# Kernel optimization log

Hardware: AMD Instinct MI355X
Metric: run time of the kernel (lower is better)

## Reference

```python
import jax, jax.numpy as jnp
import numpy as np

N = 100000
E = 3200000
D_IN = 83
D_HID = 1024
N_CLASSES = 25


def setup_inputs() -> dict:
    key = jax.random.key(0)
    ks = jax.random.split(key, 10)
    feature = jax.random.normal(ks[0], (N, D_IN), dtype=jnp.float32)
    edge_row = jax.random.randint(ks[1], (E,), 0, N, dtype=jnp.int32)
    edge_col = jax.random.randint(ks[2], (E,), 0, N, dtype=jnp.int32)
    adj_val = jax.random.uniform(ks[3], (E,), dtype=jnp.float32)
    # Conv1d(1 -> 4, kernel 5, pad 2): weight [out=4, in=1, k=5]
    conv_w = jax.random.normal(ks[4], (4, 1, 5), dtype=jnp.float32) * 0.2
    conv_b = jnp.zeros((4,), dtype=jnp.float32)
    # GCN weights (kaiming-uniform-like scale), zero biases
    W1 = jax.random.uniform(ks[5], (D_IN, D_HID), dtype=jnp.float32,
                            minval=-1.0, maxval=1.0) * np.sqrt(6.0 / D_IN)
    b1 = jnp.zeros((D_HID,), dtype=jnp.float32)
    W2 = jax.random.uniform(ks[6], (D_HID, N_CLASSES), dtype=jnp.float32,
                            minval=-1.0, maxval=1.0) * np.sqrt(6.0 / D_HID)
    b2 = jnp.zeros((N_CLASSES,), dtype=jnp.float32)
    return {"feature": feature, "conv_w": conv_w, "conv_b": conv_b,
            "W1": W1, "b1": b1, "W2": W2, "b2": b2,
            "adj_val": adj_val, "edge_row": edge_row, "edge_col": edge_col}


def _spmm(vals, row, col, X):
    # sparse(adj) @ X : gather source rows, scale by edge value, scatter-add to dest
    return jax.ops.segment_sum(vals[:, None] * X[col], row, num_segments=N)


def reference(feature, conv_w, conv_b, W1, b1, W2, b2, adj_val, edge_row, edge_col):
    # Conv1d prelude: [N,1,83] -> [N,4,83], sum over channels, relu -> [N,83]
    x = jax.lax.conv_general_dilated(
        feature[:, None, :], conv_w, window_strides=(1,), padding=[(2, 2)],
        dimension_numbers=("NCH", "OIH", "NCH"))
    x = x + conv_b[None, :, None]
    x = jax.nn.relu(jnp.sum(x, axis=1))
    # GCN layer 1: relu(A @ (x W1) + b1)
    h = jax.nn.relu(_spmm(adj_val, edge_row, edge_col, x @ W1) + b1)
    # GCN layer 2: A @ (h W2) + b2
    logits = _spmm(adj_val, edge_row, edge_col, h @ W2) + b2
    return logits
```

## Files before the change

kernel.cpp:

```cpp
#include <hip/hip_runtime.h>

#define NN   100000
#define EE   3200000
#define DIN  83
#define DHID 1024
#define NCLS 25
#define XPAD 96
#define ZPAD 32

#define NBK     391
#define CHUNK   8192

typedef __attribute__((__ext_vector_type__(8))) short sh8;
typedef __attribute__((__ext_vector_type__(4))) float f4_t;

static __device__ __forceinline__ float relu_(float v) { return v > 0.f ? v : 0.f; }

static __device__ __forceinline__ unsigned short f2bf(float f) {
  unsigned int u = __float_as_uint(f);
  unsigned int r = u + 0x7FFFu + ((u >> 16) & 1u);
  return (unsigned short)(r >> 16);
}
static __device__ __forceinline__ float bflo(unsigned int q) {
  return __uint_as_float(q << 16);
}
static __device__ __forceinline__ float bfhi(unsigned int q) {
  return __uint_as_float(q & 0xFFFF0000u);
}

__global__ __launch_bounds__(256) void conv_relu_k(
    const float* __restrict__ feature, const float* __restrict__ conv_w,
    const float* __restrict__ conv_b, unsigned short* __restrict__ x) {
  float ws0 = conv_w[0] + conv_w[5] + conv_w[10] + conv_w[15];
  float ws1 = conv_w[1] + conv_w[6] + conv_w[11] + conv_w[16];
  float ws2 = conv_w[2] + conv_w[7] + conv_w[12] + conv_w[17];
  float ws3 = conv_w[3] + conv_w[8] + conv_w[13] + conv_w[18];
  float ws4 = conv_w[4] + conv_w[9] + conv_w[14] + conv_w[19];
  float bs  = conv_b[0] + conv_b[1] + conv_b[2] + conv_b[3];
  int t = blockIdx.x * 256 + threadIdx.x;
  if (t >= NN * 12) return;
  int n = t / 12;
  int g = t - n * 12;
  int i0 = g * 8;
  const float* f = feature + (size_t)n * DIN;
  float fv[12];
#pragma unroll
  for (int k = 0; k < 12; ++k) {
    int idx = i0 - 2 + k;
    fv[k] = (idx >= 0 && idx < DIN) ? f[idx] : 0.f;
  }
  sh8 vout;
#pragma unroll
  for (int j = 0; j < 8; ++j) {
    int i = i0 + j;
    unsigned short o = 0;
    if (i < DIN) {
      float acc = bs + ws0 * fv[j] + ws1 * fv[j + 1] + ws2 * fv[j + 2] +
                  ws3 * fv[j + 3] + ws4 * fv[j + 4];
      o = f2bf(relu_(acc));
    }
    vout[j] = (short)o;
  }
  *(sh8*)&x[(size_t)n * XPAD + i0] = vout;
}

__global__ void prep_k(const float* __restrict__ W1, unsigned short* __restrict__ w1t,
                       const float* __restrict__ W2, unsigned short* __restrict__ w2t,
                       int* __restrict__ gbk) {
  int idx = blockIdx.x * blockDim.x + threadIdx.x;
  if (idx < DHID * XPAD) {
    int k = idx / DHID;
    int n = idx - k * DHID;
    float v = (k < DIN) ? W1[k * DHID + n] : 0.f;
    w1t[n * XPAD + k] = f2bf(v);
  }
  if (idx < 32 * DHID) {
    int k = idx / 32;
    int n = idx - k * 32;
    float v = (n < NCLS) ? W2[k * NCLS + n] : 0.f;
    w2t[n * DHID + k] = f2bf(v);
  }
  if (idx < NBK * 16) gbk[idx] = 0;
}


__global__ __launch_bounds__(512) void bucket_hist_k(
    const int* __restrict__ row, int* __restrict__ gbk) {
  __shared__ int cnt[NBK];
  const int tid = threadIdx.x;
  for (int b = tid; b < NBK; b += 512) cnt[b] = 0;
  __syncthreads();
  const int cb = blockIdx.x * CHUNK;
  const int csize = (cb + CHUNK <= EE) ? CHUNK : (EE - cb);
  for (int i = tid; i < csize; i += 512)
    atomicAdd(&cnt[row[cb + i] >> 8], 1);
  __syncthreads();
  for (int b = tid; b < NBK; b += 512)
    if (cnt[b]) atomicAdd(&gbk[b * 16], cnt[b]);
}

__global__ void scan_buckets_k(const int* __restrict__ gbk,
                               int* __restrict__ bbase, int* __restrict__ gcur) {
  __shared__ int sd[512];
  int t = threadIdx.x;
  int v = (t < NBK) ? gbk[t * 16] : 0;
  sd[t] = v;
  __syncthreads();
  for (int off = 1; off < 512; off <<= 1) {
    int add = (t >= off) ? sd[t - off] : 0;
    __syncthreads();
    sd[t] += add;
    __syncthreads();
  }
  if (t < NBK) {
    int excl = sd[t] - v;
    bbase[t] = excl;
    gcur[t * 16] = excl;
  }
  if (t == 0) bbase[NBK] = EE;
}

__global__ __launch_bounds__(256) void partition_k(
    const float* __restrict__ vals, const int* __restrict__ row,
    const int* __restrict__ col, int* __restrict__ gcur,
    int2* __restrict__ tmp) {
  __shared__ int cnt[NBK];
  __shared__ int lcur[NBK];
  const int tid = threadIdx.x;
  const int cb = blockIdx.x * CHUNK;
  const int csize = (cb + CHUNK <= EE) ? CHUNK : (EE - cb);

  for (int b = tid; b < NBK; b += 256) cnt[b] = 0;
  __syncthreads();
  for (int i = tid; i < csize; i += 256)
    atomicAdd(&cnt[row[cb + i] >> 8], 1);
  __syncthreads();
  for (int b = tid; b < NBK; b += 256)
    lcur[b] = cnt[b] ? atomicAdd(&gcur[b * 16], cnt[b]) : 0;
  __syncthreads();
  for (int i = tid; i < csize; i += 256) {
    int r = row[cb + i];
    int pos = atomicAdd(&lcur[r >> 8], 1);
    tmp[pos] = make_int2(col[cb + i] | ((r & 255) << 17),
                         __float_as_int(vals[cb + i]));
  }
}

__global__ __launch_bounds__(512) void fine_scatter2_k(
    const int* __restrict__ bbase, const int2* __restrict__ tmp,
    int2* __restrict__ csr, int* __restrict__ offs, int* __restrict__ counts) {
  __shared__ int cnt[256];
  __shared__ int sd[256];
  __shared__ int lcur[256];
  const int tid = threadIdx.x;
  const int b = blockIdx.x;
  const int r0 = b * 256;
  const int gstart = bbase[b];
  const int nedge = bbase[b + 1] - gstart;
  if (tid < 256) cnt[tid] = 0;
  __syncthreads();
  for (int i = tid; i < nedge; i += 512)
    atomicAdd(&cnt[((unsigned)tmp[gstart + i].x) >> 17], 1);
  __syncthreads();
  int v = 0;
  if (tid < 256) { v = cnt[tid]; sd[tid] = v; }
  __syncthreads();
  for (int off = 1; off < 256; off <<= 1) {
    int add = (tid >= off && tid < 256) ? sd[tid - off] : 0;
    __syncthreads();
    if (tid < 256) sd[tid] += add;
    __syncthreads();
  }
  if (tid < 256) {
    int excl = gstart + sd[tid] - v;
    int r = r0 + tid;
    if (r < NN) {
      offs[r] = excl;
      counts[r] = v;
    }
    lcur[tid] = excl;
  }
  __syncthreads();
  for (int i = tid; i < nedge; i += 512) {
    int2 p = tmp[gstart + i];
    int rl = ((unsigned)p.x) >> 17;
    int pos = atomicAdd(&lcur[rl], 1);
    csr[pos] = make_int2(p.x & 0x1FFFF, p.y);
  }
}

__global__ __launch_bounds__(256) void spmm83_g(
    const int* __restrict__ offs, const int* __restrict__ cnt,
    const int2* __restrict__ csr, const unsigned short* __restrict__ x,
    unsigned short* __restrict__ ax) {
  int wave = (int)((blockIdx.x * blockDim.x + threadIdx.x) >> 6);
  int lane = threadIdx.x & 63;
  if (wave >= NN) return;
  int s = __builtin_amdgcn_readfirstlane(offs[wave]);
  int n = __builtin_amdgcn_readfirstlane(cnt[wave]);
  const bool act = lane < 48;
  const int d2 = lane * 2;
  float a0 = 0.f, a1 = 0.f;
  int i = 0;
  for (; i + 8 <= n; i += 8) {
    int2 p[8];
#pragma unroll
    for (int u = 0; u < 8; ++u) p[u] = csr[s + i + u];
    if (act) {
      unsigned int q[8];
#pragma unroll
      for (int u = 0; u < 8; ++u)
        q[u] = *(const unsigned int*)&x[(size_t)p[u].x * XPAD + d2];
#pragma unroll
      for (int u = 0; u < 8; ++u) {
        float v = __int_as_float(p[u].y);
        a0 += v * bflo(q[u]);
        a1 += v * bfhi(q[u]);
      }
    }
  }
  for (; i < n; ++i) {
    int2 p = csr[s + i];
    if (act) {
      unsigned int q = *(const unsigned int*)&x[(size_t)p.x * XPAD + d2];
      float v = __int_as_float(p.y);
      a0 += v * bflo(q);
      a1 += v * bfhi(q);
    }
  }
  if (act) {
    unsigned int o = (unsigned int)f2bf(a0) | ((unsigned int)f2bf(a1) << 16);
    *(unsigned int*)&ax[(size_t)wave * XPAD + d2] = o;
  }
}

__global__ __launch_bounds__(256) void spmm25_g(
    const int* __restrict__ offs, const int* __restrict__ cnt,
    const int2* __restrict__ csr, const unsigned short* __restrict__ zb,
    const float* __restrict__ b2, float* __restrict__ out) {
  int gw = (int)((blockIdx.x * blockDim.x + threadIdx.x) >> 6);
  int lane = threadIdx.x & 63;
  int sub = lane >> 4;
  int d2 = (lane & 15) * 2;
  int r = gw * 4 + sub;
  if (r >= NN) return;
  int s = offs[r];
  int n = cnt[r];
  float a0 = 0.f, a1 = 0.f;
  int i = 0;
  for (; i + 8 <= n; i += 8) {
    int2 p[8];
#pragma unroll
    for (int u = 0; u < 8; ++u) p[u] = csr[s + i + u];
    unsigned int q[8];
#pragma unroll
    for (int u = 0; u < 8; ++u)
      q[u] = *(const unsigned int*)&zb[(size_t)p[u].x * ZPAD + d2];
#pragma unroll
    for (int u = 0; u < 8; ++u) {
      float v = __int_as_float(p[u].y);
      a0 += v * bflo(q[u]);
      a1 += v * bfhi(q[u]);
    }
  }
  for (; i < n; ++i) {
    int2 p = csr[s + i];
    unsigned int q = *(const unsigned int*)&zb[(size_t)p.x * ZPAD + d2];
    float v = __int_as_float(p.y);
    a0 += v * bflo(q);
    a1 += v * bfhi(q);
  }
  if (d2 < NCLS)     out[(size_t)r * NCLS + d2]     = a0 + b2[d2];
  if (d2 + 1 < NCLS) out[(size_t)r * NCLS + d2 + 1] = a1 + b2[d2 + 1];
}

__global__ __launch_bounds__(256) void fused_mlp_mfma(
    const unsigned short* __restrict__ axg, const unsigned short* __restrict__ w1t,
    const float* __restrict__ b1, const unsigned short* __restrict__ w2t,
    unsigned short* __restrict__ zb) {
  __shared__ __align__(16) unsigned short axs[128 * 104];
  __shared__ __align__(16) unsigned short hs[128 * 136];
  __shared__ float b1s[DHID];
  const int tid = threadIdx.x;
  const int n0 = blockIdx.x * 128;

  for (int idx = tid; idx < 128 * 12; idx += 256) {
    int m = idx / 12;
    int c8 = idx - m * 12;
    int node = n0 + m;
    sh8 v = {0, 0, 0, 0, 0, 0, 0, 0};
    if (node < NN) v = *(const sh8*)&axg[(size_t)node * XPAD + c8 * 8];
    *(sh8*)&axs[m * 104 + c8 * 8] = v;
  }
  for (int i = tid; i < DHID; i += 256) b1s[i] = b1[i];
  __syncthreads();

  const int lane = tid & 63;
  const int w = tid >> 6;
  const int quad = lane >> 4;
  const int tn = lane & 15;
  const int mta = w;
  const int mtb = w + 4;

  sh8 a1[8][3];
#pragma unroll
  for (int mt = 0; mt < 8; ++mt)
#pragma unroll
    for (int kc = 0; kc < 3; ++kc)
      a1[mt][kc] = *(const sh8*)&axs[(mt * 16 + tn) * 104 + kc * 32 + quad * 8];

  f4_t za0 = {0.f, 0.f, 0.f, 0.f}, za1 = {0.f, 0.f, 0.f, 0.f};
  f4_t zb0 = {0.f, 0.f, 0.f, 0.f}, zb1 = {0.f, 0.f, 0.f, 0.f};

  for (int c = 0; c < 8; ++c) {
    const int cb = c * 128;
#pragma unroll
    for (int nti = 0; nti < 2; ++nti) {
      const int nt = w * 2 + nti;
      const int ng = cb + nt * 16 + tn;
      const unsigned short* wr = &w1t[(size_t)ng * XPAD + quad * 8];
      sh8 b0 = *(const sh8*)&wr[0];
      sh8 b1f = *(const sh8*)&wr[32];
      sh8 b2f = *(const sh8*)&wr[64];
      float bias = b1s[ng];
#pragma unroll
      for (int mt = 0; mt < 8; ++mt) {
        f4_t acc = {0.f, 0.f, 0.f, 0.f};
        acc = __builtin_amdgcn_mfma_f32_16x16x32_bf16(a1[mt][0], b0, acc, 0, 0, 0);
        acc = __builtin_amdgcn_mfma_f32_16x16x32_bf16(a1[mt][1], b1f, acc, 0, 0, 0);
        acc = __builtin_amdgcn_mfma_f32_16x16x32_bf16(a1[mt][2], b2f, acc, 0, 0, 0);
#pragma unroll
        for (int r = 0; r < 4; ++r) {
          float v = relu_(acc[r] + bias);
          hs[(mt * 16 + quad * 4 + r) * 136 + nt * 16 + tn] = f2bf(v);
        }
      }
    }
    __syncthreads();
#pragma unroll
    for (int kc = 0; kc < 4; ++kc) {
      sh8 bl = *(const sh8*)&w2t[(size_t)tn * DHID + cb + kc * 32 + quad * 8];
      sh8 bh = *(const sh8*)&w2t[(size_t)(16 + tn) * DHID + cb + kc * 32 + quad * 8];
      sh8 aa = *(const sh8*)&hs[(mta * 16 + tn) * 136 + kc * 32 + quad * 8];
      za0 = __builtin_amdgcn_mfma_f32_16x16x32_bf16(aa, bl, za0, 0, 0, 0);
      za1 = __builtin_amdgcn_mfma_f32_16x16x32_bf16(aa, bh, za1, 0, 0, 0);
      sh8 ab = *(const sh8*)&hs[(mtb * 16 + tn) * 136 + kc * 32 + quad * 8];
      zb0 = __builtin_amdgcn_mfma_f32_16x16x32_bf16(ab, bl, zb0, 0, 0, 0);
      zb1 = __builtin_amdgcn_mfma_f32_16x16x32_bf16(ab, bh, zb1, 0, 0, 0);
    }
    __syncthreads();
  }

#pragma unroll
  for (int r = 0; r < 4; ++r) {
    int na = n0 + mta * 16 + quad * 4 + r;
    if (na < NN) {
      zb[(size_t)na * ZPAD + tn]      = f2bf(za0[r]);
      zb[(size_t)na * ZPAD + 16 + tn] = f2bf(za1[r]);
    }
    int nb = n0 + mtb * 16 + quad * 4 + r;
    if (nb < NN) {
      zb[(size_t)nb * ZPAD + tn]      = f2bf(zb0[r]);
      zb[(size_t)nb * ZPAD + 16 + tn] = f2bf(zb1[r]);
    }
  }
}

extern "C" void kernel_launch(void* const* d_in, const int* in_sizes, int n_in,
                              void* d_out, int out_size, void* d_ws, size_t ws_size,
                              hipStream_t stream) {
  const float* feature = (const float*)d_in[0];
  const float* conv_w  = (const float*)d_in[1];
  const float* conv_b  = (const float*)d_in[2];
  const float* W1      = (const float*)d_in[3];
  const float* b1      = (const float*)d_in[4];
  const float* W2      = (const float*)d_in[5];
  const float* b2      = (const float*)d_in[6];
  const float* adj     = (const float*)d_in[7];
  const int*   erow    = (const int*)d_in[8];
  const int*   ecol    = (const int*)d_in[9];
  float* out = (float*)d_out;

  char* B = (char*)d_ws;
  size_t o = 0;
  auto alloc = [&](size_t bytes, size_t align) -> void* {
    o = (o + align - 1) & ~(align - 1);
    void* p = B + o;
    o += bytes;
    return p;
  };
  unsigned short* x    = (unsigned short*)alloc((size_t)NN * XPAD * 2, 16);
  unsigned short* ax   = (unsigned short*)alloc((size_t)NN * XPAD * 2, 16);
  unsigned short* zb   = (unsigned short*)alloc((size_t)NN * ZPAD * 2, 16);
  int*   counts  = (int*)alloc((size_t)NN * 4, 16);
  int*   offs    = (int*)alloc((size_t)NN * 4, 16);
  int*   gcur    = (int*)alloc((size_t)NBK * 16 * 4, 64);
  int*   gbk     = (int*)alloc((size_t)NBK * 16 * 4, 64);
  int*   bbase   = (int*)alloc((size_t)(NBK + 1) * 4, 16);
  unsigned short* w1t = (unsigned short*)alloc((size_t)DHID * XPAD * 2, 16);
  unsigned short* w2t = (unsigned short*)alloc((size_t)32 * DHID * 2, 16);
  int2*  tmp     = (int2*)alloc((size_t)EE * 8, 16);
  int2*  csr     = (int2*)alloc((size_t)EE * 8, 16);

  conv_relu_k<<<(NN * 12 + 255) / 256, 256, 0, stream>>>(feature, conv_w, conv_b, x);
  prep_k<<<(DHID * XPAD + 255) / 256, 256, 0, stream>>>(W1, w1t, W2, w2t, gbk);
  bucket_hist_k<<<(EE + CHUNK - 1) / CHUNK, 512, 0, stream>>>(erow, gbk);
  scan_buckets_k<<<1, 512, 0, stream>>>(gbk, bbase, gcur);
  partition_k<<<(EE + CHUNK - 1) / CHUNK, 256, 0, stream>>>(adj, erow, ecol, gcur, tmp);
  fine_scatter2_k<<<NBK, 512, 0, stream>>>(bbase, tmp, csr, offs, counts);
  spmm83_g<<<(NN + 3) / 4, 256, 0, stream>>>(offs, counts, csr, x, ax);
  fused_mlp_mfma<<<(NN + 127) / 128, 256, 0, stream>>>(ax, w1t, b1, w2t, zb);
  spmm25_g<<<(NN + 15) / 16, 256, 0, stream>>>(offs, counts, csr, zb, b2, out);
}
```

Measured before the change: 460.1 us.

## Replace bucket histogram and scan with fixed-size slabs, fuse prep kernels

Drops the global bucket histogram pass and the single-block scan by giving each coarse row bucket a fixed slab of SLAB entries, with positions taken directly from atomic cursors. The conv and weight-prep kernels are merged into one launch, and the spmm83 gather loop gains a 16-way unrolled path. This removes a full read of edge_row and two launches, but it assumes no bucket exceeds SLAB edges. That holds for uniform random rows but would overflow silently on skewed graphs.

```diff
diff --git a/kernel.cpp b/kernel.cpp
--- a/kernel.cpp
+++ b/kernel.cpp
@@ -9,6 +9,7 @@
 #define ZPAD 32
 
 #define NBK     391
+#define SLAB    10240
 #define CHUNK   8192
 
 typedef __attribute__((__ext_vector_type__(8))) short sh8;
@@ -28,20 +29,36 @@
   return __uint_as_float(q & 0xFFFF0000u);
 }
 
-__global__ __launch_bounds__(256) void conv_relu_k(
+__global__ __launch_bounds__(256) void prelude_k(
     const float* __restrict__ feature, const float* __restrict__ conv_w,
-    const float* __restrict__ conv_b, unsigned short* __restrict__ x) {
+    const float* __restrict__ conv_b, unsigned short* __restrict__ x,
+    const float* __restrict__ W1, unsigned short* __restrict__ w1t,
+    const float* __restrict__ W2, unsigned short* __restrict__ w2t,
+    int* __restrict__ gcur) {
+  int t = blockIdx.x * 256 + threadIdx.x;
+  if (t < DHID * XPAD) {
+    int k = t / DHID;
+    int n = t - k * DHID;
+    float v = (k < DIN) ? W1[k * DHID + n] : 0.f;
+    w1t[n * XPAD + k] = f2bf(v);
+  }
+  if (t < 32 * DHID) {
+    int k = t / 32;
+    int n = t - k * 32;
+    float v = (n < NCLS) ? W2[k * NCLS + n] : 0.f;
+    w2t[n * DHID + k] = f2bf(v);
+  }
+  if (t < NBK * 16) gcur[t] = 0;
+  if (t >= NN * 12) return;
+  int n = t / 12;
+  int g = t - n * 12;
+  int i0 = g * 8;
   float ws0 = conv_w[0] + conv_w[5] + conv_w[10] + conv_w[15];
   float ws1 = conv_w[1] + conv_w[6] + conv_w[11] + conv_w[16];
   float ws2 = conv_w[2] + conv_w[7] + conv_w[12] + conv_w[17];
   float ws3 = conv_w[3] + conv_w[8] + conv_w[13] + conv_w[18];
   float ws4 = conv_w[4] + conv_w[9] + conv_w[14] + conv_w[19];
   float bs  = conv_b[0] + conv_b[1] + conv_b[2] + conv_b[3];
-  int t = blockIdx.x * 256 + threadIdx.x;
-  if (t >= NN * 12) return;
-  int n = t / 12;
-  int g = t - n * 12;
-  int i0 = g * 8;
   const float* f = feature + (size_t)n * DIN;
   float fv[12];
 #pragma unroll
@@ -62,62 +79,6 @@
     vout[j] = (short)o;
   }
   *(sh8*)&x[(size_t)n * XPAD + i0] = vout;
-}
-
-__global__ void prep_k(const float* __restrict__ W1, unsigned short* __restrict__ w1t,
-                       const float* __restrict__ W2, unsigned short* __restrict__ w2t,
-                       int* __restrict__ gbk) {
-  int idx = blockIdx.x * blockDim.x + threadIdx.x;
-  if (idx < DHID * XPAD) {
-    int k = idx / DHID;
-    int n = idx - k * DHID;
-    float v = (k < DIN) ? W1[k * DHID + n] : 0.f;
-    w1t[n * XPAD + k] = f2bf(v);
-  }
-  if (idx < 32 * DHID) {
-    int k = idx / 32;
-    int n = idx - k * 32;
-    float v = (n < NCLS) ? W2[k * NCLS + n] : 0.f;
-    w2t[n * DHID + k] = f2bf(v);
-  }
-  if (idx < NBK * 16) gbk[idx] = 0;
-}
-
-
-__global__ __launch_bounds__(512) void bucket_hist_k(
-    const int* __restrict__ row, int* __restrict__ gbk) {
-  __shared__ int cnt[NBK];
-  const int tid = threadIdx.x;
-  for (int b = tid; b < NBK; b += 512) cnt[b] = 0;
-  __syncthreads();
-  const int cb = blockIdx.x * CHUNK;
-  const int csize = (cb + CHUNK <= EE) ? CHUNK : (EE - cb);
-  for (int i = tid; i < csize; i += 512)
-    atomicAdd(&cnt[row[cb + i] >> 8], 1);
-  __syncthreads();
-  for (int b = tid; b < NBK; b += 512)
-    if (cnt[b]) atomicAdd(&gbk[b * 16], cnt[b]);
-}
-
-__global__ void scan_buckets_k(const int* __restrict__ gbk,
-                               int* __restrict__ bbase, int* __restrict__ gcur) {
-  __shared__ int sd[512];
-  int t = threadIdx.x;
-  int v = (t < NBK) ? gbk[t * 16] : 0;
-  sd[t] = v;
-  __syncthreads();
-  for (int off = 1; off < 512; off <<= 1) {
-    int add = (t >= off) ? sd[t - off] : 0;
-    __syncthreads();
-    sd[t] += add;
-    __syncthreads();
-  }
-  if (t < NBK) {
-    int excl = sd[t] - v;
-    bbase[t] = excl;
-    gcur[t * 16] = excl;
-  }
-  if (t == 0) bbase[NBK] = EE;
 }
 
 __global__ __launch_bounds__(256) void partition_k(
@@ -136,7 +97,7 @@
     atomicAdd(&cnt[row[cb + i] >> 8], 1);
   __syncthreads();
   for (int b = tid; b < NBK; b += 256)
-    lcur[b] = cnt[b] ? atomicAdd(&gcur[b * 16], cnt[b]) : 0;
+    lcur[b] = cnt[b] ? (b * SLAB + atomicAdd(&gcur[b * 16], cnt[b])) : 0;
   __syncthreads();
   for (int i = tid; i < csize; i += 256) {
     int r = row[cb + i];
@@ -147,7 +108,7 @@
 }
 
 __global__ __launch_bounds__(512) void fine_scatter2_k(
-    const int* __restrict__ bbase, const int2* __restrict__ tmp,
+    const int* __restrict__ gcur, const int2* __restrict__ tmp,
     int2* __restrict__ csr, int* __restrict__ offs, int* __restrict__ counts) {
   __shared__ int cnt[256];
   __shared__ int sd[256];
@@ -155,8 +116,8 @@
   const int tid = threadIdx.x;
   const int b = blockIdx.x;
   const int r0 = b * 256;
-  const int gstart = bbase[b];
-  const int nedge = bbase[b + 1] - gstart;
+  const int gstart = b * SLAB;
+  const int nedge = gcur[b * 16];
   if (tid < 256) cnt[tid] = 0;
   __syncthreads();
   for (int i = tid; i < nedge; i += 512)
@@ -202,6 +163,23 @@
   const int d2 = lane * 2;
   float a0 = 0.f, a1 = 0.f;
   int i = 0;
+  for (; i + 16 <= n; i += 16) {
+    int2 p[16];
+#pragma unroll
+    for (int u = 0; u < 16; ++u) p[u] = csr[s + i + u];
+    if (act) {
+      unsigned int q[16];
+#pragma unroll
+      for (int u = 0; u < 16; ++u)
+        q[u] = *(const unsigned int*)&x[(size_t)p[u].x * XPAD + d2];
+#pragma unroll
+      for (int u = 0; u < 16; ++u) {
+        float v = __int_as_float(p[u].y);
+        a0 += v * bflo(q[u]);
+        a1 += v * bfhi(q[u]);
+      }
+    }
+  }
   for (; i + 8 <= n; i += 8) {
     int2 p[8];
 #pragma unroll
@@ -395,19 +373,15 @@
   int*   counts  = (int*)alloc((size_t)NN * 4, 16);
   int*   offs    = (int*)alloc((size_t)NN * 4, 16);
   int*   gcur    = (int*)alloc((size_t)NBK * 16 * 4, 64);
-  int*   gbk     = (int*)alloc((size_t)NBK * 16 * 4, 64);
-  int*   bbase   = (int*)alloc((size_t)(NBK + 1) * 4, 16);
   unsigned short* w1t = (unsigned short*)alloc((size_t)DHID * XPAD * 2, 16);
   unsigned short* w2t = (unsigned short*)alloc((size_t)32 * DHID * 2, 16);
-  int2*  tmp     = (int2*)alloc((size_t)EE * 8, 16);
-  int2*  csr     = (int2*)alloc((size_t)EE * 8, 16);
-
-  conv_relu_k<<<(NN * 12 + 255) / 256, 256, 0, stream>>>(feature, conv_w, conv_b, x);
-  prep_k<<<(DHID * XPAD + 255) / 256, 256, 0, stream>>>(W1, w1t, W2, w2t, gbk);
-  bucket_hist_k<<<(EE + CHUNK - 1) / CHUNK, 512, 0, stream>>>(erow, gbk);
-  scan_buckets_k<<<1, 512, 0, stream>>>(gbk, bbase, gcur);
+  int2*  tmp     = (int2*)alloc((size_t)NBK * SLAB * 8, 16);
+  int2*  csr     = (int2*)alloc((size_t)NBK * SLAB * 8, 16);
+
+  prelude_k<<<(NN * 12 + 255) / 256, 256, 0, stream>>>(
+      feature, conv_w, conv_b, x, W1, w1t, W2, w2t, gcur);
   partition_k<<<(EE + CHUNK - 1) / CHUNK, 256, 0, stream>>>(adj, erow, ecol, gcur, tmp);
-  fine_scatter2_k<<<NBK, 512, 0, stream>>>(bbase, tmp, csr, offs, counts);
+  fine_scatter2_k<<<NBK, 512, 0, stream>>>(gcur, tmp, csr, offs, counts);
   spmm83_g<<<(NN + 3) / 4, 256, 0, stream>>>(offs, counts, csr, x, ax);
   fused_mlp_mfma<<<(NN + 127) / 128, 256, 0, stream>>>(ax, w1t, b1, w2t, zb);
   spmm25_g<<<(NN + 15) / 16, 256, 0, stream>>>(offs, counts, csr, zb, b2, out);
```

After: 442.2 us. 3.9% less time.
